# Kernel optimization log

Measured on AMD Instinct MI355X. Metric: run time of the kernel, lower is better.

Reference implementation:

```python
import jax, jax.numpy as jnp
import numpy as np

GROUPS = 32
EPS = 1e-5
NUM_HEADS = 8


def group_norm(x, gamma, beta):
    B, C, H, W = x.shape
    xg = x.reshape(B, GROUPS, C // GROUPS, H, W)
    mean = xg.mean(axis=(2, 3, 4), keepdims=True)
    var = xg.var(axis=(2, 3, 4), keepdims=True)
    xg = (xg - mean) * jax.lax.rsqrt(var + EPS)
    x = xg.reshape(B, C, H, W)
    return x * gamma[None, :, None, None] + beta[None, :, None, None]


def setup_inputs() -> dict:
    key = jax.random.key(0)
    k1, k2, k3 = jax.random.split(key, 3)
    C = 512
    x = jax.random.normal(k1, (16, C, 32, 32), dtype=jnp.float32)
    gn_gamma = jnp.ones((C,), dtype=jnp.float32)
    gn_beta = jnp.zeros((C,), dtype=jnp.float32)
    w_qkv = jax.random.normal(k2, (3 * C, C), dtype=jnp.float32) * 0.02
    b_qkv = jnp.zeros((3 * C,), dtype=jnp.float32)
    w_proj = jax.random.normal(k3, (C, C), dtype=jnp.float32) * 0.02
    b_proj = jnp.zeros((C,), dtype=jnp.float32)
    return {"x": x, "gn_gamma": gn_gamma, "gn_beta": gn_beta,
            "w_qkv": w_qkv, "b_qkv": b_qkv, "w_proj": w_proj, "b_proj": b_proj}


def reference(x, gn_gamma, gn_beta, w_qkv, b_qkv, w_proj, b_proj):
    B, C, H, W = x.shape
    nh = NUM_HEADS
    hd = C // nh
    h = group_norm(x, gn_gamma, gn_beta)
    # 1x1 conv == channel matmul: [B,3C,H,W]
    qkv = jnp.einsum('bchw,oc->bohw', h, w_qkv) + b_qkv[None, :, None, None]
    qkv = qkv.reshape(B, 3, nh, hd, H * W)
    q, k, v = qkv[:, 0], qkv[:, 1], qkv[:, 2]  # [B, nh, hd, HW]
    scale = hd ** -0.5
    # attn[b,n,i,j] = sum_d q[b,n,d,i] * k[b,n,d,j]
    attn = jax.nn.softmax(jnp.einsum('bndi,bndj->bnij', q, k) * scale, axis=-1)
    # h[b,n,d,i] = sum_j v[b,n,d,j] * attn[b,n,i,j]
    h = jnp.einsum('bndj,bnij->bndi', v, attn).reshape(B, C, H, W)
    out = jnp.einsum('bchw,oc->bohw', h, w_proj) + b_proj[None, :, None, None]
    return x + out
```

## Files before the change

kernel.cpp:

```cpp
#include <hip/hip_runtime.h>

typedef __bf16 bf16;
typedef __bf16 bf16x4 __attribute__((ext_vector_type(4)));
typedef __bf16 bf16x8 __attribute__((ext_vector_type(8)));
typedef float  f32x4  __attribute__((ext_vector_type(4)));

#define MFMA(a,b,c) __builtin_amdgcn_mfma_f32_16x16x32_bf16((a),(b),(c),0,0,0)

__device__ __forceinline__ void gll16(const void* g, void* l) {
  __builtin_amdgcn_global_load_lds((const __attribute__((address_space(1))) unsigned int*)g,
                                   (__attribute__((address_space(3))) unsigned int*)l, 16, 0, 0);
}

static constexpr int Cc = 512;
static constexpr int Ss = 1024;
#define QSCALE 0.18033688011112042f

__global__ __launch_bounds__(256) void k_wconv(const float* __restrict__ wq, const float* __restrict__ wp,
                                               bf16* __restrict__ wqb, bf16* __restrict__ wpb) {
  const int i = blockIdx.x * 256 + threadIdx.x;
  if (i * 4 < 786432) {
    float4 v = ((const float4*)wq)[i];
    bf16x4 o = { (bf16)v.x, (bf16)v.y, (bf16)v.z, (bf16)v.w };
    ((bf16x4*)wqb)[i] = o;
  } else {
    const int j = i - 786432 / 4;
    float4 v = ((const float4*)wp)[j];
    bf16x4 o = { (bf16)v.x, (bf16)v.y, (bf16)v.z, (bf16)v.w };
    ((bf16x4*)wpb)[j] = o;
  }
}

__global__ __launch_bounds__(256) void k_gnorm(const float* __restrict__ x,
                                               const float* __restrict__ gamma,
                                               const float* __restrict__ beta,
                                               bf16* __restrict__ ht) {
  const int g = blockIdx.x;
  const int b = blockIdx.y;
  const float* base = x + ((size_t)b * Cc + g * 16) * Ss;
  const int tid = threadIdx.x;

  float s = 0.f, sq = 0.f;
  const float4* b4 = (const float4*)base;
  for (int i = tid; i < 4096; i += 256) {
    float4 v = b4[i];
    s  += v.x + v.y + v.z + v.w;
    sq += v.x * v.x + v.y * v.y + v.z * v.z + v.w * v.w;
  }
  #pragma unroll
  for (int m = 1; m < 64; m <<= 1) { s += __shfl_xor(s, m); sq += __shfl_xor(sq, m); }
  __shared__ float red[8];
  if ((tid & 63) == 0) { red[tid >> 6] = s; red[4 + (tid >> 6)] = sq; }
  __syncthreads();
  const float stot = red[0] + red[1] + red[2] + red[3];
  const float sqt  = red[4] + red[5] + red[6] + red[7];
  const float mean = stot * (1.f / 16384.f);
  const float var  = sqt * (1.f / 16384.f) - mean * mean;
  const float rstd = rsqrtf(var + 1e-5f);

  float gm[16], bt[16];
  #pragma unroll
  for (int c = 0; c < 16; ++c) {
    const float gv = gamma[g * 16 + c] * rstd;
    gm[c] = gv;
    bt[c] = beta[g * 16 + c] - mean * gv;
  }
  bf16* dst0 = ht + (size_t)b * Ss * Cc + g * 16;
  for (int sI = tid; sI < 1024; sI += 256) {
    bf16x8 o0, o1;
    #pragma unroll
    for (int c = 0; c < 8; ++c) o0[c] = (bf16)(base[c * 1024 + sI] * gm[c] + bt[c]);
    #pragma unroll
    for (int c = 0; c < 8; ++c) o1[c] = (bf16)(base[(8 + c) * 1024 + sI] * gm[8 + c] + bt[8 + c]);
    bf16* d = dst0 + (size_t)sI * Cc;
    *(bf16x8*)d = o0;
    *(bf16x8*)(d + 8) = o1;
  }
}

template<int MODE>
__global__ __launch_bounds__(256) void k_gemm(const bf16* __restrict__ Aw,
                                              const bf16* __restrict__ Bt,
                                              const float* __restrict__ bias,
                                              bf16* __restrict__ qo, bf16* __restrict__ ko,
                                              bf16* __restrict__ vo,
                                              const float* __restrict__ xres,
                                              float* __restrict__ out) {
  const int nt = blockIdx.x, mt = blockIdx.y, b = blockIdx.z;
  const int M0 = mt * 128, N0 = nt * 128;
  __shared__ __align__(16) bf16 lA[128 * 64];
  __shared__ __align__(16) bf16 lB[128 * 64];
  const int tid = threadIdx.x;
  const int l = tid & 63, w = tid >> 6;
  const int wm = w >> 1, wn = w & 1;
  const int l15 = l & 15, gq = l >> 4;
  const bf16* Bb = Bt + (size_t)b * Ss * Cc;
  const int rowS = tid >> 3;
  const int cb = (tid & 7) * 16;

  f32x4 acc[4][4];
  #pragma unroll
  for (int i = 0; i < 4; ++i)
    #pragma unroll
    for (int j = 0; j < 4; ++j) acc[i][j] = f32x4{0.f, 0.f, 0.f, 0.f};

  for (int kt = 0; kt < 8; ++kt) {
    #pragma unroll
    for (int p = 0; p < 4; ++p) {
      const int r = p * 32 + rowS;
      gll16((const char*)Aw + ((size_t)(M0 + r) * 512 + kt * 64) * 2 + cb,
            (char*)lA + p * 4096 + tid * 16);
    }
    #pragma unroll
    for (int p = 0; p < 4; ++p) {
      const int r = p * 32 + rowS;
      gll16((const char*)Bb + ((size_t)(N0 + r) * 512 + kt * 64) * 2 + cb,
            (char*)lB + p * 4096 + tid * 16);
    }
    __syncthreads();
    #pragma unroll
    for (int kk = 0; kk < 2; ++kk) {
      bf16x8 af[4], bfr[4];
      #pragma unroll
      for (int mf = 0; mf < 4; ++mf)
        af[mf] = *(const bf16x8*)((const char*)lA + (wm * 64 + mf * 16 + l15) * 128 + kk * 64 + gq * 16);
      #pragma unroll
      for (int nf = 0; nf < 4; ++nf)
        bfr[nf] = *(const bf16x8*)((const char*)lB + (wn * 64 + nf * 16 + l15) * 128 + kk * 64 + gq * 16);
      #pragma unroll
      for (int mf = 0; mf < 4; ++mf)
        #pragma unroll
        for (int nf = 0; nf < 4; ++nf)
          acc[mf][nf] = MFMA(af[mf], bfr[nf], acc[mf][nf]);
    }
    __syncthreads();
  }

  #pragma unroll
  for (int mf = 0; mf < 4; ++mf) {
    const int ofr = M0 + wm * 64 + mf * 16;
    float bi[4];
    #pragma unroll
    for (int r = 0; r < 4; ++r) bi[r] = bias[ofr + gq * 4 + r];
    #pragma unroll
    for (int nf = 0; nf < 4; ++nf) {
      const int sI = N0 + wn * 64 + nf * 16 + l15;
      f32x4 v = acc[mf][nf];
      if (MODE == 0) {
        const int which = ofr >> 9;
        const int nh = (ofr >> 6) & 7;
        const int dbase = (ofr & 63) + gq * 4;
        const size_t bh = (size_t)b * 8 + nh;
        if (which == 2) {
          #pragma unroll
          for (int r = 0; r < 4; ++r)
            vo[(bh * 64 + dbase + r) * 1024 + sI] = (bf16)(v[r] + bi[r]);
        } else {
          const float qs = which ? 1.f : QSCALE;
          bf16x4 pk = { (bf16)((v[0] + bi[0]) * qs), (bf16)((v[1] + bi[1]) * qs),
                        (bf16)((v[2] + bi[2]) * qs), (bf16)((v[3] + bi[3]) * qs) };
          bf16* dst = (which ? ko : qo) + (bh * 1024 + sI) * 64 + dbase;
          *(bf16x4*)dst = pk;
        }
      } else {
        #pragma unroll
        for (int r = 0; r < 4; ++r) {
          const size_t idx = ((size_t)b * 512 + ofr + gq * 4 + r) * 1024 + sI;
          out[idx] = xres[idx] + bi[r] + v[r];
        }
      }
    }
  }
}

__global__ __launch_bounds__(512, 4) void k_attn(const bf16* __restrict__ qT,
                                                 const bf16* __restrict__ kT,
                                                 const bf16* __restrict__ vv,
                                                 bf16* __restrict__ ao) {
  const int it = blockIdx.x, nh = blockIdx.y, b = blockIdx.z;
  const size_t bh = (size_t)b * 8 + nh;
  const char* kh = (const char*)(kT + bh * 65536);
  const char* vh = (const char*)(vv + bh * 65536);
  __shared__ __align__(16) char smem[49152];
  const int tid = threadIdx.x;
  const int w = tid >> 6, l = tid & 63;
  const int l15 = l & 15, g = l >> 4;
  char* lpw = smem + 32768 + w * 2048;
  const int swq = (l15 & 7) << 4;

  const int rowS = tid >> 3;
  const int cb = (tid & 7) * 16;
  const int sw = cb ^ ((rowS & 7) << 4);
  const char* ksrc = kh + rowS * 128 + sw;
  const char* vsrc = vh + rowS * 2048 + sw;

  gll16(ksrc, smem + tid * 16);
  gll16(vsrc, smem + 16384 + tid * 16);

  const bf16* qrow = qT + bh * 65536 + (size_t)(it * 128 + w * 16 + l15) * 64;
  const bf16x8 aq0 = *(const bf16x8*)(qrow + g * 8);
  const bf16x8 aq1 = *(const bf16x8*)(qrow + 32 + g * 8);

  const bf16 one1 = (bf16)1.0f;
  const bf16x8 vone = { one1, one1, one1, one1, one1, one1, one1, one1 };

  f32x4 oacc[4];
  #pragma unroll
  for (int df = 0; df < 4; ++df) oacc[df] = f32x4{0.f, 0.f, 0.f, 0.f};
  f32x4 oext = f32x4{0.f, 0.f, 0.f, 0.f};

  __syncthreads();

  int cur = 0;
  for (int t = 0; t < 16; ++t) {
    if (t < 15) {
      gll16(ksrc + (t + 1) * 8192, smem + (cur ^ 1) * 8192 + tid * 16);
      gll16(vsrc + (t + 1) * 128, smem + 16384 + (cur ^ 1) * 8192 + tid * 16);
    }
    const char* lkc = smem + cur * 8192;
    const char* lvc = smem + 16384 + cur * 8192;

    f32x4 sf[4];
    #pragma unroll
    for (int nf = 0; nf < 4; ++nf) sf[nf] = f32x4{0.f, 0.f, 0.f, 0.f};
    __builtin_amdgcn_s_setprio(1);
    #pragma unroll
    for (int kk = 0; kk < 2; ++kk) {
      const bf16x8 aq = kk ? aq1 : aq0;
      #pragma unroll
      for (int nf = 0; nf < 4; ++nf) {
        const int r = nf * 16 + l15;
        bf16x8 bk = *(const bf16x8*)(lkc + r * 128 + ((kk * 64 + g * 16) ^ ((r & 7) << 4)));
        sf[nf] = MFMA(bk, aq, sf[nf]);
      }
    }
    __builtin_amdgcn_s_setprio(0);
    #pragma unroll
    for (int nf = 0; nf < 4; ++nf) {
      const float p0 = exp2f(sf[nf][0]), p1 = exp2f(sf[nf][1]),
                  p2 = exp2f(sf[nf][2]), p3 = exp2f(sf[nf][3]);
      bf16x4 pk = { (bf16)p0, (bf16)p1, (bf16)p2, (bf16)p3 };
      *(bf16x4*)(lpw + l15 * 128 + ((nf * 32 + g * 8) ^ swq)) = pk;
    }
    const bf16x8 pa0 = *(const bf16x8*)(lpw + l15 * 128 + ((g * 16) ^ swq));
    const bf16x8 pa1 = *(const bf16x8*)(lpw + l15 * 128 + ((64 + g * 16) ^ swq));
    __builtin_amdgcn_s_setprio(1);
    oext = MFMA(pa0, vone, oext);
    oext = MFMA(pa1, vone, oext);
    #pragma unroll
    for (int jj = 0; jj < 2; ++jj) {
      const bf16x8 pa = jj ? pa1 : pa0;
      #pragma unroll
      for (int df = 0; df < 4; ++df) {
        const int r = df * 16 + l15;
        bf16x8 bv = *(const bf16x8*)(lvc + r * 128 + ((jj * 64 + g * 16) ^ ((r & 7) << 4)));
        oacc[df] = MFMA(pa, bv, oacc[df]);
      }
    }
    __builtin_amdgcn_s_setprio(0);
    __syncthreads();
    cur ^= 1;
  }

  float rinv[4];
  #pragma unroll
  for (int r = 0; r < 4; ++r) rinv[r] = 1.f / oext[r];
  #pragma unroll
  for (int df = 0; df < 4; ++df) {
    #pragma unroll
    for (int r = 0; r < 4; ++r) {
      const int i = it * 128 + w * 16 + g * 4 + r;
      ao[((size_t)b * 1024 + i) * 512 + nh * 64 + df * 16 + l15] = (bf16)(oacc[df][r] * rinv[r]);
    }
  }
}

extern "C" void kernel_launch(void* const* d_in, const int* in_sizes, int n_in,
                              void* d_out, int out_size, void* d_ws, size_t ws_size,
                              hipStream_t stream) {
  (void)in_sizes; (void)n_in; (void)out_size; (void)ws_size;
  const float* x   = (const float*)d_in[0];
  const float* gam = (const float*)d_in[1];
  const float* bet = (const float*)d_in[2];
  const float* wq  = (const float*)d_in[3];
  const float* bq  = (const float*)d_in[4];
  const float* wp  = (const float*)d_in[5];
  const float* bp  = (const float*)d_in[6];
  float* out = (float*)d_out;

  bf16* ws  = (bf16*)d_ws;
  bf16* ht  = ws;
  bf16* qT  = ws + 8388608;
  bf16* kT  = ws + 16777216;
  bf16* vv  = ws + 25165824;
  bf16* wqb = ws + 33554432;
  bf16* wpb = ws + 34340864;

  k_wconv<<<1024, 256, 0, stream>>>(wq, wp, wqb, wpb);
  k_gnorm<<<dim3(32, 16), 256, 0, stream>>>(x, gam, bet, ht);
  k_gemm<0><<<dim3(8, 12, 16), 256, 0, stream>>>(wqb, ht, bq, qT, kT, vv, nullptr, nullptr);
  k_attn<<<dim3(8, 8, 16), 512, 0, stream>>>(qT, kT, vv, ht);
  k_gemm<1><<<dim3(8, 4, 16), 256, 0, stream>>>(wpb, ht, bp, nullptr, nullptr, nullptr, x, out);
}
```

Measured before the change: 154.5 us.

## Triple-buffer attention K/V loads with explicit vmcnt waits; register-cache groupnorm input

The attention kernel moves from a double buffer to a three-stage LDS ring for K/V tiles. It prefetches two tiles ahead, replaces the end-of-iteration __syncthreads with an explicit s_waitcnt vmcnt plus a barrier, and precomputes the swizzled LDS offsets. Groupnorm now keeps each thread's 16 float4 values in registers, so x is read from global memory once instead of twice, and the output is written as contiguous channel-last rows. The costs are 64KB of LDS per attention block, which may cut occupancy, and higher register pressure in groupnorm.

```diff
diff --git a/kernel.cpp b/kernel.cpp
--- a/kernel.cpp
+++ b/kernel.cpp
@@ -31,21 +31,22 @@
   }
 }
 
-__global__ __launch_bounds__(256) void k_gnorm(const float* __restrict__ x,
-                                               const float* __restrict__ gamma,
-                                               const float* __restrict__ beta,
-                                               bf16* __restrict__ ht) {
+__global__ __launch_bounds__(256, 2) void k_gnorm(const float* __restrict__ x,
+                                                  const float* __restrict__ gamma,
+                                                  const float* __restrict__ beta,
+                                                  bf16* __restrict__ ht) {
   const int g = blockIdx.x;
   const int b = blockIdx.y;
   const float* base = x + ((size_t)b * Cc + g * 16) * Ss;
   const int tid = threadIdx.x;
 
+  f32x4 xr[16];
   float s = 0.f, sq = 0.f;
-  const float4* b4 = (const float4*)base;
-  for (int i = tid; i < 4096; i += 256) {
-    float4 v = b4[i];
-    s  += v.x + v.y + v.z + v.w;
-    sq += v.x * v.x + v.y * v.y + v.z * v.z + v.w * v.w;
+  #pragma unroll
+  for (int k = 0; k < 16; ++k) {
+    xr[k] = ((const f32x4*)base)[k * 256 + tid];
+    s  += xr[k][0] + xr[k][1] + xr[k][2] + xr[k][3];
+    sq += xr[k][0] * xr[k][0] + xr[k][1] * xr[k][1] + xr[k][2] * xr[k][2] + xr[k][3] * xr[k][3];
   }
   #pragma unroll
   for (int m = 1; m < 64; m <<= 1) { s += __shfl_xor(s, m); sq += __shfl_xor(sq, m); }
@@ -58,21 +59,22 @@
   const float var  = sqt * (1.f / 16384.f) - mean * mean;
   const float rstd = rsqrtf(var + 1e-5f);
 
-  float gm[16], bt[16];
-  #pragma unroll
-  for (int c = 0; c < 16; ++c) {
-    const float gv = gamma[g * 16 + c] * rstd;
-    gm[c] = gv;
-    bt[c] = beta[g * 16 + c] - mean * gv;
-  }
-  bf16* dst0 = ht + (size_t)b * Ss * Cc + g * 16;
-  for (int sI = tid; sI < 1024; sI += 256) {
+  float ga[16], bb[16];
+  #pragma unroll
+  for (int k = 0; k < 16; ++k) {
+    ga[k] = gamma[g * 16 + k] * rstd;
+    bb[k] = beta[g * 16 + k] - mean * ga[k];
+  }
+
+  bf16* dst0 = ht + ((size_t)b * Ss + tid * 4) * Cc + g * 16;
+  #pragma unroll
+  for (int j = 0; j < 4; ++j) {
     bf16x8 o0, o1;
     #pragma unroll
-    for (int c = 0; c < 8; ++c) o0[c] = (bf16)(base[c * 1024 + sI] * gm[c] + bt[c]);
-    #pragma unroll
-    for (int c = 0; c < 8; ++c) o1[c] = (bf16)(base[(8 + c) * 1024 + sI] * gm[8 + c] + bt[8 + c]);
-    bf16* d = dst0 + (size_t)sI * Cc;
+    for (int k = 0; k < 8; ++k)  o0[k] = (bf16)(xr[k][j] * ga[k] + bb[k]);
+    #pragma unroll
+    for (int k = 0; k < 8; ++k)  o1[k] = (bf16)(xr[8 + k][j] * ga[8 + k] + bb[8 + k]);
+    bf16* d = dst0 + (size_t)j * Cc;
     *(bf16x8*)d = o0;
     *(bf16x8*)(d + 8) = o1;
   }
@@ -181,11 +183,11 @@
   const size_t bh = (size_t)b * 8 + nh;
   const char* kh = (const char*)(kT + bh * 65536);
   const char* vh = (const char*)(vv + bh * 65536);
-  __shared__ __align__(16) char smem[49152];
+  __shared__ __align__(16) char smem[65536];
   const int tid = threadIdx.x;
   const int w = tid >> 6, l = tid & 63;
   const int l15 = l & 15, g = l >> 4;
-  char* lpw = smem + 32768 + w * 2048;
+  char* lpw = smem + 49152 + w * 2048;
   const int swq = (l15 & 7) << 4;
 
   const int rowS = tid >> 3;
@@ -193,14 +195,32 @@
   const int sw = cb ^ ((rowS & 7) << 4);
   const char* ksrc = kh + rowS * 128 + sw;
   const char* vsrc = vh + rowS * 2048 + sw;
-
-  gll16(ksrc, smem + tid * 16);
-  gll16(vsrc, smem + 16384 + tid * 16);
+  char* lkdst = smem + tid * 16;
+  char* lvdst = smem + 24576 + tid * 16;
 
   const bf16* qrow = qT + bh * 65536 + (size_t)(it * 128 + w * 16 + l15) * 64;
   const bf16x8 aq0 = *(const bf16x8*)(qrow + g * 8);
   const bf16x8 aq1 = *(const bf16x8*)(qrow + 32 + g * 8);
 
+  int offR[2][4];
+  #pragma unroll
+  for (int kk = 0; kk < 2; ++kk)
+    #pragma unroll
+    for (int nf = 0; nf < 4; ++nf) {
+      const int r = nf * 16 + l15;
+      offR[kk][nf] = r * 128 + ((kk * 64 + g * 16) ^ ((r & 7) << 4));
+    }
+  int offPw[4];
+  #pragma unroll
+  for (int nf = 0; nf < 4; ++nf) offPw[nf] = l15 * 128 + ((nf * 32 + g * 8) ^ swq);
+  const int offPr0 = l15 * 128 + ((g * 16) ^ swq);
+  const int offPr1 = l15 * 128 + ((64 + g * 16) ^ swq);
+
+  gll16(ksrc, lkdst);
+  gll16(vsrc, lvdst);
+  gll16(ksrc + 8192, lkdst + 8192);
+  gll16(vsrc + 128, lvdst + 8192);
+
   const bf16 one1 = (bf16)1.0f;
   const bf16x8 vone = { one1, one1, one1, one1, one1, one1, one1, one1 };
 
@@ -209,16 +229,19 @@
   for (int df = 0; df < 4; ++df) oacc[df] = f32x4{0.f, 0.f, 0.f, 0.f};
   f32x4 oext = f32x4{0.f, 0.f, 0.f, 0.f};
 
-  __syncthreads();
-
-  int cur = 0;
+  int scur = 0;
   for (int t = 0; t < 16; ++t) {
-    if (t < 15) {
-      gll16(ksrc + (t + 1) * 8192, smem + (cur ^ 1) * 8192 + tid * 16);
-      gll16(vsrc + (t + 1) * 128, smem + 16384 + (cur ^ 1) * 8192 + tid * 16);
-    }
-    const char* lkc = smem + cur * 8192;
-    const char* lvc = smem + 16384 + cur * 8192;
+    if (t < 15) asm volatile("s_waitcnt vmcnt(2)" ::: "memory");
+    else        asm volatile("s_waitcnt vmcnt(0)" ::: "memory");
+    __builtin_amdgcn_s_barrier();
+    __builtin_amdgcn_sched_barrier(0);
+    if (t <= 13) {
+      const int sn = (scur == 0) ? 2 : scur - 1;
+      gll16(ksrc + (t + 2) * 8192, lkdst + sn * 8192);
+      gll16(vsrc + (t + 2) * 128, lvdst + sn * 8192);
+    }
+    const char* lkc = smem + scur * 8192;
+    const char* lvc = smem + 24576 + scur * 8192;
 
     f32x4 sf[4];
     #pragma unroll
@@ -229,8 +252,7 @@
       const bf16x8 aq = kk ? aq1 : aq0;
       #pragma unroll
       for (int nf = 0; nf < 4; ++nf) {
-        const int r = nf * 16 + l15;
-        bf16x8 bk = *(const bf16x8*)(lkc + r * 128 + ((kk * 64 + g * 16) ^ ((r & 7) << 4)));
+        bf16x8 bk = *(const bf16x8*)(lkc + offR[kk][nf]);
         sf[nf] = MFMA(bk, aq, sf[nf]);
       }
     }
@@ -240,10 +262,10 @@
       const float p0 = exp2f(sf[nf][0]), p1 = exp2f(sf[nf][1]),
                   p2 = exp2f(sf[nf][2]), p3 = exp2f(sf[nf][3]);
       bf16x4 pk = { (bf16)p0, (bf16)p1, (bf16)p2, (bf16)p3 };
-      *(bf16x4*)(lpw + l15 * 128 + ((nf * 32 + g * 8) ^ swq)) = pk;
-    }
-    const bf16x8 pa0 = *(const bf16x8*)(lpw + l15 * 128 + ((g * 16) ^ swq));
-    const bf16x8 pa1 = *(const bf16x8*)(lpw + l15 * 128 + ((64 + g * 16) ^ swq));
+      *(bf16x4*)(lpw + offPw[nf]) = pk;
+    }
+    const bf16x8 pa0 = *(const bf16x8*)(lpw + offPr0);
+    const bf16x8 pa1 = *(const bf16x8*)(lpw + offPr1);
     __builtin_amdgcn_s_setprio(1);
     oext = MFMA(pa0, vone, oext);
     oext = MFMA(pa1, vone, oext);
@@ -252,14 +274,12 @@
       const bf16x8 pa = jj ? pa1 : pa0;
       #pragma unroll
       for (int df = 0; df < 4; ++df) {
-        const int r = df * 16 + l15;
-        bf16x8 bv = *(const bf16x8*)(lvc + r * 128 + ((jj * 64 + g * 16) ^ ((r & 7) << 4)));
+        bf16x8 bv = *(const bf16x8*)(lvc + offR[jj][df]);
         oacc[df] = MFMA(pa, bv, oacc[df]);
       }
     }
     __builtin_amdgcn_s_setprio(0);
-    __syncthreads();
-    cur ^= 1;
+    scur = (scur == 2) ? 0 : scur + 1;
   }
 
   float rinv[4];
```

After: 151.2 us. -2.1%, faster.
